# Performance work log

Measured on AMD Instinct MI355X. Metric: run time of the kernel, lower is better.

## Reference

```python
import jax, jax.numpy as jnp
import numpy as np

B, H, W, C = 64, 32, 32, 384          # batch, spatial resolution, channels
NH, WS = 12, 7                        # num_heads, window_size
HD = C // NH                          # head_dim = key_dim (attn_ratio=1)
MLP_H = 4 * C                         # mlp_ratio=4
SCALE = HD ** -0.5
EPS = 1e-5


def _bias_idxs():
    # replicate Attention.__init__ relative-position index construction
    pts = [(i, j) for i in range(WS) for j in range(WS)]
    offs, idxs = {}, []
    for p1 in pts:
        for p2 in pts:
            o = (abs(p1[0] - p2[0]), abs(p1[1] - p2[1]))
            if o not in offs:
                offs[o] = len(offs)
            idxs.append(offs[o])
    return np.array(idxs, dtype=np.int32).reshape(WS * WS, WS * WS), len(offs)


def setup_inputs() -> dict:
    key = jax.random.key(0)
    ks = jax.random.split(key, 8)
    idxs, n_off = _bias_idxs()
    s = lambda k, shape: jax.random.normal(k, shape, jnp.float32) * 0.02
    return {
        'x': jax.random.normal(ks[0], (B, H * W, C), jnp.float32),
        'ln1_g': jnp.ones((C,), jnp.float32), 'ln1_b': jnp.zeros((C,), jnp.float32),
        'qkv_w': s(ks[1], (C, 3 * C)), 'qkv_b': jnp.zeros((3 * C,), jnp.float32),
        'proj_w': s(ks[2], (C, C)), 'proj_b': jnp.zeros((C,), jnp.float32),
        'attn_biases': s(ks[3], (NH, n_off)),
        'conv_w': s(ks[4], (C, 1, 3, 3)),
        'bn_g': jnp.ones((C,), jnp.float32), 'bn_b': jnp.zeros((C,), jnp.float32),
        'bn_m': jnp.zeros((C,), jnp.float32), 'bn_v': jnp.ones((C,), jnp.float32),
        'ln2_g': jnp.ones((C,), jnp.float32), 'ln2_b': jnp.zeros((C,), jnp.float32),
        'fc1_w': s(ks[5], (C, MLP_H)), 'fc1_b': jnp.zeros((MLP_H,), jnp.float32),
        'fc2_w': s(ks[6], (MLP_H, C)), 'fc2_b': jnp.zeros((C,), jnp.float32),
        'bias_idxs': jnp.asarray(idxs),
    }


def _ln(x, g, b):
    m = x.mean(-1, keepdims=True)
    v = ((x - m) ** 2).mean(-1, keepdims=True)
    return (x - m) * jax.lax.rsqrt(v + EPS) * g + b


def _block(x, ln1_g, ln1_b, qkv_w, qkv_b, proj_w, proj_b, attn_biases,
           conv_w, bn_g, bn_b, bn_m, bn_v, ln2_g, ln2_b,
           fc1_w, fc1_b, fc2_w, fc2_b, bias_idxs):
    Bb, L, Cc = x.shape
    res = x
    # ---- window partition with padding ----
    xi = x.reshape(Bb, H, W, Cc)
    pad_b = (WS - H % WS) % WS
    pad_r = (WS - W % WS) % WS
    xi = jnp.pad(xi, ((0, 0), (0, pad_b), (0, pad_r), (0, 0)))
    pH, pW = H + pad_b, W + pad_r
    nHw, nWw = pH // WS, pW // WS
    xw = (xi.reshape(Bb, nHw, WS, nWw, WS, Cc)
            .transpose(0, 1, 3, 2, 4, 5)
            .reshape(Bb * nHw * nWw, WS * WS, Cc))
    # ---- windowed attention with gathered relative-position bias ----
    Bw, N, _ = xw.shape
    xn = _ln(xw, ln1_g, ln1_b)
    qkv = (xn @ qkv_w + qkv_b).reshape(Bw, N, NH, 3 * HD)
    q, k, v = jnp.split(qkv, 3, axis=-1)              # each [Bw, N, NH, HD]
    ab = attn_biases[:, bias_idxs]                     # gather -> [NH, N, N]
    attn = jnp.einsum('bnhd,bmhd->bhnm', q, k) * SCALE + ab
    attn = jax.nn.softmax(attn, axis=-1)
    aw = jnp.einsum('bhnm,bmhd->bnhd', attn, v).reshape(Bw, N, Cc)
    aw = aw @ proj_w + proj_b
    # ---- window merge / unpad ----
    xi = (aw.reshape(Bb, nHw, nWw, WS, WS, Cc)
            .transpose(0, 1, 3, 2, 4, 5)
            .reshape(Bb, pH, pW, Cc))[:, :H, :W]
    x = res + xi.reshape(Bb, L, Cc)
    # ---- depthwise 3x3 conv + BN (eval semantics), NCHW ----
    xc = x.transpose(0, 2, 1).reshape(Bb, Cc, H, W)
    xc = jax.lax.conv_general_dilated(xc, conv_w, (1, 1), ((1, 1), (1, 1)),
                                      feature_group_count=Cc)
    xc = ((xc - bn_m[:, None, None]) * jax.lax.rsqrt(bn_v[:, None, None] + 1e-5)
          * bn_g[:, None, None] + bn_b[:, None, None])
    x = xc.reshape(Bb, Cc, L).transpose(0, 2, 1)
    # ---- MLP (LayerNorm -> fc1 -> GELU -> fc2), residual ----
    h = jax.nn.gelu(_ln(x, ln2_g, ln2_b) @ fc1_w + fc1_b, approximate=False)
    return x + (h @ fc2_w + fc2_b)


def reference(x, ln1_g, ln1_b, qkv_w, qkv_b, proj_w, proj_b, attn_biases,
              conv_w, bn_g, bn_b, bn_m, bn_v, ln2_g, ln2_b,
              fc1_w, fc1_b, fc2_w, fc2_b, bias_idxs):
    return _block(x, ln1_g, ln1_b, qkv_w, qkv_b, proj_w, proj_b, attn_biases,
                  conv_w, bn_g, bn_b, bn_m, bn_v, ln2_g, ln2_b,
                  fc1_w, fc1_b, fc2_w, fc2_b, bias_idxs)
```

## Files before the change

### kernel.cpp

```cpp
#include <hip/hip_runtime.h>
#include <hip/hip_bf16.h>
#include <math.h>

#define NHEAD 12
#define CDIM 384
#define QKVC 1152
#define MLPH 1536
#define SCALE 0.17677669529663687f

typedef __attribute__((ext_vector_type(8))) short short8;
typedef __attribute__((ext_vector_type(4))) float f32x4;

static __device__ __forceinline__ unsigned short f2bf(float f) {
  union { __hip_bfloat16 b; unsigned short u; } c;
  c.b = __float2bfloat16(f);
  return c.u;
}

static __device__ __forceinline__ float gelu_f(float x) {
  float x3 = x * x * x;
  float y = 0.7978845608028654f * (x + 0.044715f * x3);
  float e = __expf(2.f * y);
  float th = 1.f - 2.f / (e + 1.f);
  return 0.5f * x * (1.f + th);
}

__global__ void pad_qkv_kernel(const float* __restrict__ lb, const float* __restrict__ Wq,
                               const float* __restrict__ bq, __hip_bfloat16* __restrict__ outp) {
  int j = blockIdx.x * blockDim.x + threadIdx.x;
  if (j >= QKVC) return;
  float s = bq[j];
  for (int c = 0; c < CDIM; c++) s += lb[c] * Wq[(size_t)c * QKVC + j];
  outp[j] = __float2bfloat16(s);
}

__global__ void expand_bias(const float* __restrict__ biases, const int* __restrict__ bidx,
                            float* __restrict__ Bexp, int n_off) {
  int h = blockIdx.x;
  for (int e = threadIdx.x; e < 4096; e += 256) {
    int n = e >> 6, m = e & 63;
    float v;
    if (m >= 49) v = -1e30f;
    else if (n >= 49) v = 0.f;
    else v = biases[h * n_off + bidx[n * 49 + m]];
    Bexp[h * 4096 + e] = v;
  }
}

__global__ void wt_convert(const float* __restrict__ W, __hip_bfloat16* __restrict__ Wt,
                           int K, int N) {
  __shared__ float t[32][33];
  int n0 = blockIdx.x * 32, k0 = blockIdx.y * 32;
  int tx = threadIdx.x, ty = threadIdx.y;
#pragma unroll
  for (int i = 0; i < 4; i++) t[ty + i * 8][tx] = W[(size_t)(k0 + ty + i * 8) * N + n0 + tx];
  __syncthreads();
#pragma unroll
  for (int i = 0; i < 4; i++)
    Wt[(size_t)(n0 + ty + i * 8) * K + k0 + tx] = __float2bfloat16(t[tx][ty + i * 8]);
}

__global__ void wfragq(const float* __restrict__ W, unsigned short* __restrict__ WF) {
  int f = blockIdx.x;
  int lane = threadIdx.x;
  int kk = f % 12, G = f / 12;
  int n = G * 16 + (lane & 15);
  int k = kk * 32 + (lane >> 4) * 8;
  unsigned short* dst = WF + ((size_t)f * 64 + lane) * 8;
#pragma unroll
  for (int j = 0; j < 8; j++) dst[j] = f2bf(W[(size_t)(k + j) * QKVC + n]);
}

__global__ void wfrag1(const float* __restrict__ W, unsigned short* __restrict__ WF) {
  int f = blockIdx.x;
  int lane = threadIdx.x;
  int wn = f & 7, kk = (f >> 3) % 12, ks = f / 96;
  int n = ks * 128 + wn * 16 + (lane & 15);
  int k = kk * 32 + (lane >> 4) * 8;
  unsigned short* dst = WF + ((size_t)f * 64 + lane) * 8;
#pragma unroll
  for (int j = 0; j < 8; j++) dst[j] = f2bf(W[(size_t)(k + j) * MLPH + n]);
}

__global__ void wfrag2(const float* __restrict__ W, unsigned short* __restrict__ WF) {
  int f = blockIdx.x;
  int lane = threadIdx.x;
  int j = f % 3, wn = (f / 3) & 7, kk = (f / 24) & 3, ks = f / 96;
  int n = wn * 48 + j * 16 + (lane & 15);
  int k = ks * 128 + kk * 32 + (lane >> 4) * 8;
  unsigned short* dst = WF + ((size_t)f * 64 + lane) * 8;
#pragma unroll
  for (int jj = 0; jj < 8; jj++) dst[jj] = f2bf(W[(size_t)(k + jj) * CDIM + n]);
}

__global__ __launch_bounds__(512) void ln_qkv(
    const float* __restrict__ X, const float* __restrict__ g, const float* __restrict__ b,
    const unsigned short* __restrict__ WQF, const float* __restrict__ BQ,
    __hip_bfloat16* __restrict__ QKV) {
  __shared__ unsigned short Al[64][388];
  int tid = threadIdx.x;
  int m0 = blockIdx.x * 64;
  int wave = tid >> 6, lane = tid & 63;
  int l15 = lane & 15, l4 = lane >> 4;

#pragma unroll
  for (int r8 = 0; r8 < 8; r8++) {
    int row = wave * 8 + r8;
    const float* xr = X + (size_t)(m0 + row) * CDIM;
    float vals[6];
    float s = 0.f;
#pragma unroll
    for (int i = 0; i < 6; i++) { vals[i] = xr[lane + i * 64]; s += vals[i]; }
#pragma unroll
    for (int o = 32; o > 0; o >>= 1) s += __shfl_xor(s, o);
    float mean = s * (1.f / 384.f);
    float vs = 0.f;
#pragma unroll
    for (int i = 0; i < 6; i++) { float d = vals[i] - mean; vs += d * d; }
#pragma unroll
    for (int o = 32; o > 0; o >>= 1) vs += __shfl_xor(vs, o);
    float rs = rsqrtf(vs * (1.f / 384.f) + 1e-5f);
#pragma unroll
    for (int i = 0; i < 6; i++) {
      int c = lane + i * 64;
      Al[row][c] = f2bf((vals[i] - mean) * rs * g[c] + b[c]);
    }
  }
  __syncthreads();

  for (int rd = 0; rd < 9; rd++) {
    int G = rd * 8 + wave;
    f32x4 acc[4] = {};
    const unsigned short* wb = WQF + (size_t)(G * 12) * 512 + lane * 8;
#pragma unroll
    for (int kk = 0; kk < 12; kk++) {
      short8 bf = *(const short8*)(wb + kk * 512);
#pragma unroll
      for (int i = 0; i < 4; i++) {
        short8 af = *(const short8*)&Al[i * 16 + l15][kk * 32 + l4 * 8];
        acc[i] = __builtin_amdgcn_mfma_f32_16x16x32_bf16(af, bf, acc[i], 0, 0, 0);
      }
    }
    int n = G * 16 + l15;
    float bv = BQ[n];
    __hip_bfloat16* dst = QKV + (size_t)m0 * QKVC + n;
#pragma unroll
    for (int i = 0; i < 4; i++)
#pragma unroll
      for (int r = 0; r < 4; r++)
        dst[(size_t)(i * 16 + l4 * 4 + r) * QKVC] = __float2bfloat16(acc[i][r] + bv);
  }
}

template <int GELU, int HAS_RES, int OUT_BF16>
__global__ __launch_bounds__(256) void gemm_mfma(
    const __hip_bfloat16* __restrict__ A, const __hip_bfloat16* __restrict__ Bt,
    const float* __restrict__ bias, const float* __restrict__ res,
    void* __restrict__ Cout, int M, int N, int K) {
  __shared__ unsigned short Al[128][72];
  __shared__ unsigned short Bl[64][72];
  int tid = threadIdx.x;
  int m0 = blockIdx.y * 128, n0 = blockIdx.x * 64;
  int wave = tid >> 6, lane = tid & 63;
  int wm = (wave >> 1) * 64, wn = (wave & 1) * 32;
  int l15 = lane & 15, l4 = lane >> 4;

  int am = tid >> 1, ak = (tid & 1) * 32;
  int bn = tid >> 2, bk = (tid & 3) * 16;
  const __hip_bfloat16* Ag = A + (size_t)(m0 + am) * K + ak;
  const __hip_bfloat16* Bg = Bt + (size_t)(n0 + bn) * K + bk;

  f32x4 acc[4][2] = {};

  for (int kt = 0; kt < K; kt += 64) {
    uint4 av0 = *(const uint4*)(Ag + kt);
    uint4 av1 = *(const uint4*)(Ag + kt + 8);
    uint4 av2 = *(const uint4*)(Ag + kt + 16);
    uint4 av3 = *(const uint4*)(Ag + kt + 24);
    uint4 bv0 = *(const uint4*)(Bg + kt);
    uint4 bv1 = *(const uint4*)(Bg + kt + 8);
    __syncthreads();
    *(uint4*)&Al[am][ak]      = av0;
    *(uint4*)&Al[am][ak + 8]  = av1;
    *(uint4*)&Al[am][ak + 16] = av2;
    *(uint4*)&Al[am][ak + 24] = av3;
    *(uint4*)&Bl[bn][bk]      = bv0;
    *(uint4*)&Bl[bn][bk + 8]  = bv1;
    __syncthreads();
#pragma unroll
    for (int kk = 0; kk < 64; kk += 32) {
      short8 af[4], bfr[2];
#pragma unroll
      for (int i = 0; i < 4; i++)
        af[i] = *(const short8*)&Al[wm + i * 16 + l15][kk + l4 * 8];
#pragma unroll
      for (int j = 0; j < 2; j++)
        bfr[j] = *(const short8*)&Bl[wn + j * 16 + l15][kk + l4 * 8];
#pragma unroll
      for (int i = 0; i < 4; i++)
#pragma unroll
        for (int j = 0; j < 2; j++)
          acc[i][j] = __builtin_amdgcn_mfma_f32_16x16x32_bf16(af[i], bfr[j], acc[i][j], 0, 0, 0);
    }
  }

#pragma unroll
  for (int i = 0; i < 4; i++) {
#pragma unroll
    for (int j = 0; j < 2; j++) {
      int n = n0 + wn + j * 16 + l15;
      float bv = bias[n];
#pragma unroll
      for (int r = 0; r < 4; r++) {
        int m = m0 + wm + i * 16 + l4 * 4 + r;
        float c = acc[i][j][r] + bv;
        if (GELU) c = gelu_f(c);
        if (HAS_RES) c += res[(size_t)m * N + n];
        if (OUT_BF16)
          ((__hip_bfloat16*)Cout)[(size_t)m * N + n] = __float2bfloat16(c);
        else
          ((float*)Cout)[(size_t)m * N + n] = c;
      }
    }
  }
}

__global__ __launch_bounds__(512, 4) void mlp_fused(
    const __hip_bfloat16* __restrict__ XN, const unsigned short* __restrict__ W1F,
    const float* __restrict__ B1, const unsigned short* __restrict__ W2F,
    const float* __restrict__ B2, const __hip_bfloat16* __restrict__ X2,
    float* __restrict__ OUT) {
  __shared__ unsigned short XNl[64][388];
  __shared__ unsigned short Hl[64][132];
  int tid = threadIdx.x;
  int m0 = blockIdx.x * 64;
  int wave = tid >> 6, lane = tid & 63;
  int wn = wave;
  int l15 = lane & 15, l4 = lane >> 4;

  {
#pragma unroll
    for (int i = 0; i < 6; i++) {
      int u = tid + i * 512;
      int r = u / 48, col = (u % 48) * 8;
      *(uint4*)&XNl[r][col] =
          *(const uint4*)((const unsigned short*)XN + (size_t)(m0 + r) * 384 + col);
    }
  }

  f32x4 acc[4][3] = {};
  __syncthreads();

  for (int ks = 0; ks < 12; ks++) {
    f32x4 hacc[4] = {};
    const unsigned short* w1fb = W1F + ((size_t)(ks * 96 + wn)) * 512 + lane * 8;
#pragma unroll
    for (int kk = 0; kk < 12; kk++) {
      short8 bf0 = *(const short8*)(w1fb + kk * 4096);
#pragma unroll
      for (int i = 0; i < 4; i++) {
        short8 af = *(const short8*)&XNl[i * 16 + l15][kk * 32 + l4 * 8];
        hacc[i] = __builtin_amdgcn_mfma_f32_16x16x32_bf16(af, bf0, hacc[i], 0, 0, 0);
      }
    }
    float b1v = B1[ks * 128 + wn * 16 + l15];
    __syncthreads();
#pragma unroll
    for (int i = 0; i < 4; i++)
#pragma unroll
      for (int r = 0; r < 4; r++) {
        float c = hacc[i][r] + b1v;
        Hl[i * 16 + l4 * 4 + r][wn * 16 + l15] = f2bf(gelu_f(c));
      }
    __syncthreads();
    const unsigned short* w2fb = W2F + ((size_t)(ks * 96 + wn * 3)) * 512 + lane * 8;
#pragma unroll
    for (int kk = 0; kk < 4; kk++) {
      short8 af2[4];
#pragma unroll
      for (int i = 0; i < 4; i++)
        af2[i] = *(const short8*)&Hl[i * 16 + l15][kk * 32 + l4 * 8];
#pragma unroll
      for (int j = 0; j < 3; j++) {
        short8 bf2 = *(const short8*)(w2fb + kk * 12288 + j * 512);
#pragma unroll
        for (int i = 0; i < 4; i++)
          acc[i][j] = __builtin_amdgcn_mfma_f32_16x16x32_bf16(af2[i], bf2, acc[i][j], 0, 0, 0);
      }
    }
  }
#pragma unroll
  for (int j = 0; j < 3; j++) {
    int n = wn * 48 + j * 16 + l15;
    float bv = B2[n];
#pragma unroll
    for (int i = 0; i < 4; i++)
#pragma unroll
      for (int r = 0; r < 4; r++) {
        int m = m0 + i * 16 + l4 * 4 + r;
        OUT[(size_t)m * 384 + n] =
            acc[i][j][r] + bv + __bfloat162float(X2[(size_t)m * 384 + n]);
      }
  }
}

__global__ __launch_bounds__(64) void attn_mfma(
    const __hip_bfloat16* __restrict__ qkv, const __hip_bfloat16* __restrict__ qkv_pad,
    const float* __restrict__ Bexp, __hip_bfloat16* __restrict__ aw) {
  int h = blockIdx.x % NHEAD;
  int w = blockIdx.x / NHEAD;
  int b = w / 25, wi = w % 25;
  int wh = wi / 5, wv = wi % 5;

  __shared__ unsigned short Q[64][40];
  __shared__ unsigned short K[64][40];
  __shared__ unsigned short Vt[32][72];
  __shared__ unsigned short P[64][72];

  int lane = threadIdx.x;
  int l15 = lane & 15, l4 = lane >> 4;

  {
    int t = lane;
    uint4 z = {0, 0, 0, 0};
    uint4 qv[4], kv[4];
    union { uint4 u[4]; unsigned short s[32]; } vu;
    bool use = t < 49;
    const unsigned short* src = (const unsigned short*)qkv_pad + h * 96;
    if (use) {
      int hh = wh * 7 + t / 7, ww = wv * 7 + t % 7;
      if (hh < 32 && ww < 32)
        src = (const unsigned short*)qkv + (size_t)(b * 1024 + hh * 32 + ww) * QKVC + h * 96;
    }
#pragma unroll
    for (int c = 0; c < 4; c++) {
      qv[c]   = use ? *(const uint4*)(src + c * 8)      : z;
      kv[c]   = use ? *(const uint4*)(src + 32 + c * 8) : z;
      vu.u[c] = use ? *(const uint4*)(src + 64 + c * 8) : z;
    }
#pragma unroll
    for (int c = 0; c < 4; c++) {
      *(uint4*)&Q[t][c * 8] = qv[c];
      *(uint4*)&K[t][c * 8] = kv[c];
    }
#pragma unroll
    for (int d = 0; d < 32; d++) Vt[d][t] = vu.s[d];
  }
  __syncthreads();

  f32x4 acc[4][4] = {};
  {
    short8 aq[4], bk[4];
#pragma unroll
    for (int i = 0; i < 4; i++) aq[i] = *(const short8*)&Q[i * 16 + l15][l4 * 8];
#pragma unroll
    for (int j = 0; j < 4; j++) bk[j] = *(const short8*)&K[j * 16 + l15][l4 * 8];
#pragma unroll
    for (int i = 0; i < 4; i++)
#pragma unroll
      for (int j = 0; j < 4; j++)
        acc[i][j] = __builtin_amdgcn_mfma_f32_16x16x32_bf16(aq[i], bk[j], acc[i][j], 0, 0, 0);
  }

  const float* Bh = Bexp + h * 4096;
  float rinv_[4][4];
#pragma unroll
  for (int i = 0; i < 4; i++) {
    float s[4][4];
#pragma unroll
    for (int j = 0; j < 4; j++)
#pragma unroll
      for (int r = 0; r < 4; r++) {
        int n = i * 16 + l4 * 4 + r, m = j * 16 + l15;
        s[j][r] = acc[i][j][r] * SCALE + Bh[n * 64 + m];
      }
#pragma unroll
    for (int r = 0; r < 4; r++) {
      float mx = fmaxf(fmaxf(s[0][r], s[1][r]), fmaxf(s[2][r], s[3][r]));
#pragma unroll
      for (int o = 1; o < 16; o <<= 1) mx = fmaxf(mx, __shfl_xor(mx, o));
      float p[4], sm = 0.f;
#pragma unroll
      for (int j = 0; j < 4; j++) { p[j] = __expf(s[j][r] - mx); sm += p[j]; }
#pragma unroll
      for (int o = 1; o < 16; o <<= 1) sm += __shfl_xor(sm, o);
      rinv_[i][r] = 1.f / sm;
      int n = i * 16 + l4 * 4 + r;
#pragma unroll
      for (int j = 0; j < 4; j++) P[n][j * 16 + l15] = f2bf(p[j]);
    }
  }
  __syncthreads();

  f32x4 o[4][2] = {};
#pragma unroll
  for (int ks = 0; ks < 2; ks++) {
    short8 pa[4], vb[2];
#pragma unroll
    for (int i = 0; i < 4; i++) pa[i] = *(const short8*)&P[i * 16 + l15][ks * 32 + l4 * 8];
#pragma unroll
    for (int j = 0; j < 2; j++) vb[j] = *(const short8*)&Vt[j * 16 + l15][ks * 32 + l4 * 8];
#pragma unroll
    for (int i = 0; i < 4; i++)
#pragma unroll
      for (int j = 0; j < 2; j++)
        o[i][j] = __builtin_amdgcn_mfma_f32_16x16x32_bf16(pa[i], vb[j], o[i][j], 0, 0, 0);
  }

#pragma unroll
  for (int i = 0; i < 4; i++)
#pragma unroll
    for (int r = 0; r < 4; r++) {
      int n = i * 16 + l4 * 4 + r;
      if (n < 49) {
        int hh = wh * 7 + n / 7, ww = wv * 7 + n % 7;
        if (hh < 32 && ww < 32) {
          __hip_bfloat16* dst = aw + (size_t)(b * 1024 + hh * 32 + ww) * CDIM + h * 32;
          float ri = rinv_[i][r];
#pragma unroll
          for (int j = 0; j < 2; j++)
            dst[j * 16 + l15] = __float2bfloat16(o[i][j][r] * ri);
        }
      }
    }
}

__global__ __launch_bounds__(384) void conv_bn_ln_kernel(
    const __hip_bfloat16* __restrict__ X, const float* __restrict__ W9,
    const float* __restrict__ g, const float* __restrict__ bb,
    const float* __restrict__ mm, const float* __restrict__ vv,
    const float* __restrict__ lg, const float* __restrict__ lb,
    __hip_bfloat16* __restrict__ X2, __hip_bfloat16* __restrict__ XN) {
  int nwg = gridDim.x;
  int id = blockIdx.x;
  int nid = (id & 7) * (nwg >> 3) + (id >> 3);
  int yh = nid & 1;
  int x = (nid >> 1) & 31;
  int b = nid >> 6;
  int c = threadIdx.x;

  float w[9];
#pragma unroll
  for (int i = 0; i < 9; i++) w[i] = W9[c * 9 + i];
  float bnsc = rsqrtf(vv[c] + 1e-5f) * g[c];
  float bnsh = bb[c] - mm[c] * bnsc;
  float lgc = lg[c], lbc = lb[c];

  bool xm = x > 0, xp = x < 31;
  const __hip_bfloat16* colbase = X + ((size_t)(b * 1024 + x)) * CDIM + c;

  __shared__ float part[2][6][2];
  int wv = threadIdx.x >> 6, ln = threadIdx.x & 63;

  float w0[3], w1[3], w2[3];
  int y0 = yh * 16;
  if (y0 == 0) {
    w0[0] = w0[1] = w0[2] = 0.f;
  } else {
    const __hip_bfloat16* p = colbase + (size_t)(y0 - 1) * 32 * CDIM;
    w0[0] = xm ? __bfloat162float(p[-CDIM]) : 0.f;
    w0[1] = __bfloat162float(p[0]);
    w0[2] = xp ? __bfloat162float(p[CDIM]) : 0.f;
  }
  {
    const __hip_bfloat16* p = colbase + (size_t)y0 * 32 * CDIM;
    w1[0] = xm ? __bfloat162float(p[-CDIM]) : 0.f;
    w1[1] = __bfloat162float(p[0]);
    w1[2] = xp ? __bfloat162float(p[CDIM]) : 0.f;
  }

  for (int y = y0; y < y0 + 16; y++) {
    if (y + 1 < 32) {
      const __hip_bfloat16* p = colbase + (size_t)(y + 1) * 32 * CDIM;
      w2[0] = xm ? __bfloat162float(p[-CDIM]) : 0.f;
      w2[1] = __bfloat162float(p[0]);
      w2[2] = xp ? __bfloat162float(p[CDIM]) : 0.f;
    } else {
      w2[0] = w2[1] = w2[2] = 0.f;
    }
    float acc = w0[0] * w[0] + w0[1] * w[1] + w0[2] * w[2]
              + w1[0] * w[3] + w1[1] * w[4] + w1[2] * w[5]
              + w2[0] * w[6] + w2[1] * w[7] + w2[2] * w[8];
    float r = acc * bnsc + bnsh;
    size_t tok = (size_t)(b * 1024 + y * 32 + x);
    X2[tok * CDIM + c] = __float2bfloat16(r);

    float s1 = r, s2 = r * r;
#pragma unroll
    for (int o = 32; o > 0; o >>= 1) { s1 += __shfl_xor(s1, o); s2 += __shfl_xor(s2, o); }
    int pb = y & 1;
    if (ln == 0) { part[pb][wv][0] = s1; part[pb][wv][1] = s2; }
    __syncthreads();
    float ts1 = 0.f, ts2 = 0.f;
#pragma unroll
    for (int i = 0; i < 6; i++) { ts1 += part[pb][i][0]; ts2 += part[pb][i][1]; }
    float mean = ts1 * (1.f / 384.f);
    float var = ts2 * (1.f / 384.f) - mean * mean;
    float rstd = rsqrtf(var + 1e-5f);
    XN[tok * CDIM + c] = __float2bfloat16((r - mean) * rstd * lgc + lbc);

    w0[0] = w1[0]; w0[1] = w1[1]; w0[2] = w1[2];
    w1[0] = w2[0]; w1[1] = w2[1]; w1[2] = w2[2];
  }
}

extern "C" void kernel_launch(void* const* d_in, const int* in_sizes, int n_in,
                              void* d_out, int out_size, void* d_ws, size_t ws_size,
                              hipStream_t stream) {
  const float* x      = (const float*)d_in[0];
  const float* ln1_g  = (const float*)d_in[1];
  const float* ln1_b  = (const float*)d_in[2];
  const float* qkv_w  = (const float*)d_in[3];
  const float* qkv_b  = (const float*)d_in[4];
  const float* proj_w = (const float*)d_in[5];
  const float* proj_b = (const float*)d_in[6];
  const float* att_b  = (const float*)d_in[7];
  const float* conv_w = (const float*)d_in[8];
  const float* bn_g   = (const float*)d_in[9];
  const float* bn_b   = (const float*)d_in[10];
  const float* bn_m   = (const float*)d_in[11];
  const float* bn_v   = (const float*)d_in[12];
  const float* ln2_g  = (const float*)d_in[13];
  const float* ln2_b  = (const float*)d_in[14];
  const float* fc1_w  = (const float*)d_in[15];
  const float* fc1_b  = (const float*)d_in[16];
  const float* fc2_w  = (const float*)d_in[17];
  const float* fc2_b  = (const float*)d_in[18];
  const int* bias_idxs = (const int*)d_in[19];
  int n_off = in_sizes[7] / NHEAD;
  float* out = (float*)d_out;

  char* ws = (char*)d_ws;
  size_t off = 0;
  __hip_bfloat16* qkv_pad = (__hip_bfloat16*)(ws + off); off += QKVC * 2;
  off = (off + 255) & ~(size_t)255;
  float* Bexp = (float*)(ws + off); off += (size_t)NHEAD * 4096 * 4;
  unsigned short* wqf = (unsigned short*)(ws + off); off += (size_t)QKVC * CDIM * 2;
  __hip_bfloat16* wprojT = (__hip_bfloat16*)(ws + off); off += (size_t)CDIM * CDIM * 2;
  unsigned short* w1f = (unsigned short*)(ws + off); off += (size_t)MLPH * CDIM * 2;
  unsigned short* w2f = (unsigned short*)(ws + off); off += (size_t)CDIM * MLPH * 2;
  size_t HDR = (off + 255) & ~(size_t)255;

  const size_t PER_TOK = 4608;
  int Bc = 64;
  while (Bc > 1 && HDR + (size_t)Bc * 1024 * PER_TOK > ws_size) Bc >>= 1;
  size_t Tc = (size_t)Bc * 1024;

  off = HDR;
  __hip_bfloat16* xn = (__hip_bfloat16*)(ws + off); off += Tc * CDIM * 2;
  __hip_bfloat16* qkv = (__hip_bfloat16*)(ws + off); off += Tc * QKVC * 2;
  __hip_bfloat16* x1 = qkv;
  __hip_bfloat16* awb = (__hip_bfloat16*)(ws + off); off += Tc * CDIM * 2;
  __hip_bfloat16* x2 = (__hip_bfloat16*)(ws + off); off += Tc * CDIM * 2;

  pad_qkv_kernel<<<dim3(5), dim3(256), 0, stream>>>(ln1_b, qkv_w, qkv_b, qkv_pad);
  expand_bias<<<dim3(NHEAD), dim3(256), 0, stream>>>(att_b, bias_idxs, Bexp, n_off);
  wfragq<<<dim3(864), dim3(64), 0, stream>>>(qkv_w, wqf);
  wt_convert<<<dim3(CDIM / 32, CDIM / 32), dim3(32, 8), 0, stream>>>(proj_w, wprojT, CDIM, CDIM);
  wfrag1<<<dim3(1152), dim3(64), 0, stream>>>(fc1_w, w1f);
  wfrag2<<<dim3(1152), dim3(64), 0, stream>>>(fc2_w, w2f);

  for (int b0 = 0; b0 < 64; b0 += Bc) {
    const float* xa = x + (size_t)b0 * 1024 * CDIM;
    float* outa = out + (size_t)b0 * 1024 * CDIM;
    int M = (int)Tc;

    ln_qkv<<<dim3(M / 64), dim3(512), 0, stream>>>(xa, ln1_g, ln1_b, wqf, qkv_b, qkv);
    attn_mfma<<<dim3(Bc * 25 * NHEAD), dim3(64), 0, stream>>>(qkv, qkv_pad, Bexp, awb);
    gemm_mfma<0, 1, 1><<<dim3(CDIM / 64, M / 128), dim3(256), 0, stream>>>(
        awb, wprojT, proj_b, xa, x1, M, CDIM, CDIM);
    conv_bn_ln_kernel<<<dim3(Bc * 64), dim3(384), 0, stream>>>(
        x1, conv_w, bn_g, bn_b, bn_m, bn_v, ln2_g, ln2_b, x2, xn);
    mlp_fused<<<dim3(M / 64), dim3(512), 0, stream>>>(
        xn, w1f, fc1_b, w2f, fc2_b, x2, outa);
  }
}
```

Baseline: 762.4 us.

## Replace generic proj GEMM with full-K row-block kernel using pre-fragmented weights

The projection GEMM is rewritten as a dedicated kernel: each 512-thread block loads a 64-row by 384 slab of the attention output into LDS once, then each wave computes three 16-column groups over the full K. The B operand is read directly from a pre-swizzled MFMA fragment layout in global memory. This removes the per-K-tile LDS staging and barriers, and means each A tile is read from global once instead of once per N-tile. The tanh-form GELU helper is also rewritten as an equivalent sigmoid form with fewer operations, though the proj path does not call it.

```diff
diff --git a/kernel.cpp b/kernel.cpp
--- a/kernel.cpp
+++ b/kernel.cpp
@@ -18,11 +18,10 @@
 }
 
 static __device__ __forceinline__ float gelu_f(float x) {
-  float x3 = x * x * x;
-  float y = 0.7978845608028654f * (x + 0.044715f * x3);
-  float e = __expf(2.f * y);
-  float th = 1.f - 2.f / (e + 1.f);
-  return 0.5f * x * (1.f + th);
+  float x2 = x * x;
+  float t = __builtin_fmaf(0.044715f * x2, x, x);
+  float e = __expf(-1.5957691216057308f * t);
+  return x / (1.f + e);
 }
 
 __global__ void pad_qkv_kernel(const float* __restrict__ lb, const float* __restrict__ Wq,
@@ -47,19 +46,6 @@
   }
 }
 
-__global__ void wt_convert(const float* __restrict__ W, __hip_bfloat16* __restrict__ Wt,
-                           int K, int N) {
-  __shared__ float t[32][33];
-  int n0 = blockIdx.x * 32, k0 = blockIdx.y * 32;
-  int tx = threadIdx.x, ty = threadIdx.y;
-#pragma unroll
-  for (int i = 0; i < 4; i++) t[ty + i * 8][tx] = W[(size_t)(k0 + ty + i * 8) * N + n0 + tx];
-  __syncthreads();
-#pragma unroll
-  for (int i = 0; i < 4; i++)
-    Wt[(size_t)(n0 + ty + i * 8) * K + k0 + tx] = __float2bfloat16(t[tx][ty + i * 8]);
-}
-
 __global__ void wfragq(const float* __restrict__ W, unsigned short* __restrict__ WF) {
   int f = blockIdx.x;
   int lane = threadIdx.x;
@@ -69,6 +55,17 @@
   unsigned short* dst = WF + ((size_t)f * 64 + lane) * 8;
 #pragma unroll
   for (int j = 0; j < 8; j++) dst[j] = f2bf(W[(size_t)(k + j) * QKVC + n]);
+}
+
+__global__ void wfragp(const float* __restrict__ W, unsigned short* __restrict__ WF) {
+  int f = blockIdx.x;
+  int lane = threadIdx.x;
+  int kk = f % 12, G = f / 12;
+  int n = G * 16 + (lane & 15);
+  int k = kk * 32 + (lane >> 4) * 8;
+  unsigned short* dst = WF + ((size_t)f * 64 + lane) * 8;
+#pragma unroll
+  for (int j = 0; j < 8; j++) dst[j] = f2bf(W[(size_t)(k + j) * CDIM + n]);
 }
 
 __global__ void wfrag1(const float* __restrict__ W, unsigned short* __restrict__ WF) {
@@ -152,76 +149,55 @@
   }
 }
 
-template <int GELU, int HAS_RES, int OUT_BF16>
-__global__ __launch_bounds__(256) void gemm_mfma(
-    const __hip_bfloat16* __restrict__ A, const __hip_bfloat16* __restrict__ Bt,
-    const float* __restrict__ bias, const float* __restrict__ res,
-    void* __restrict__ Cout, int M, int N, int K) {
-  __shared__ unsigned short Al[128][72];
-  __shared__ unsigned short Bl[64][72];
+__global__ __launch_bounds__(512) void proj_res(
+    const __hip_bfloat16* __restrict__ AW, const unsigned short* __restrict__ WPF,
+    const float* __restrict__ BP, const float* __restrict__ X,
+    __hip_bfloat16* __restrict__ X1) {
+  __shared__ unsigned short Al[64][388];
   int tid = threadIdx.x;
-  int m0 = blockIdx.y * 128, n0 = blockIdx.x * 64;
+  int m0 = blockIdx.x * 64;
   int wave = tid >> 6, lane = tid & 63;
-  int wm = (wave >> 1) * 64, wn = (wave & 1) * 32;
   int l15 = lane & 15, l4 = lane >> 4;
 
-  int am = tid >> 1, ak = (tid & 1) * 32;
-  int bn = tid >> 2, bk = (tid & 3) * 16;
-  const __hip_bfloat16* Ag = A + (size_t)(m0 + am) * K + ak;
-  const __hip_bfloat16* Bg = Bt + (size_t)(n0 + bn) * K + bk;
-
-  f32x4 acc[4][2] = {};
-
-  for (int kt = 0; kt < K; kt += 64) {
-    uint4 av0 = *(const uint4*)(Ag + kt);
-    uint4 av1 = *(const uint4*)(Ag + kt + 8);
-    uint4 av2 = *(const uint4*)(Ag + kt + 16);
-    uint4 av3 = *(const uint4*)(Ag + kt + 24);
-    uint4 bv0 = *(const uint4*)(Bg + kt);
-    uint4 bv1 = *(const uint4*)(Bg + kt + 8);
-    __syncthreads();
-    *(uint4*)&Al[am][ak]      = av0;
-    *(uint4*)&Al[am][ak + 8]  = av1;
-    *(uint4*)&Al[am][ak + 16] = av2;
-    *(uint4*)&Al[am][ak + 24] = av3;
-    *(uint4*)&Bl[bn][bk]      = bv0;
-    *(uint4*)&Bl[bn][bk + 8]  = bv1;
-    __syncthreads();
-#pragma unroll
-    for (int kk = 0; kk < 64; kk += 32) {
-      short8 af[4], bfr[2];
+  {
+#pragma unroll
+    for (int i = 0; i < 6; i++) {
+      int u = tid + i * 512;
+      int r = u / 48, col = (u % 48) * 8;
+      *(uint4*)&Al[r][col] =
+          *(const uint4*)((const unsigned short*)AW + (size_t)(m0 + r) * 384 + col);
+    }
+  }
+  __syncthreads();
+
+  f32x4 acc[4][3] = {};
+#pragma unroll
+  for (int kk = 0; kk < 12; kk++) {
+    short8 af[4];
+#pragma unroll
+    for (int i = 0; i < 4; i++)
+      af[i] = *(const short8*)&Al[i * 16 + l15][kk * 32 + l4 * 8];
+#pragma unroll
+    for (int j = 0; j < 3; j++) {
+      int G = wave * 3 + j;
+      short8 bf = *(const short8*)(WPF + (size_t)(G * 12 + kk) * 512 + lane * 8);
 #pragma unroll
       for (int i = 0; i < 4; i++)
-        af[i] = *(const short8*)&Al[wm + i * 16 + l15][kk + l4 * 8];
-#pragma unroll
-      for (int j = 0; j < 2; j++)
-        bfr[j] = *(const short8*)&Bl[wn + j * 16 + l15][kk + l4 * 8];
-#pragma unroll
-      for (int i = 0; i < 4; i++)
-#pragma unroll
-        for (int j = 0; j < 2; j++)
-          acc[i][j] = __builtin_amdgcn_mfma_f32_16x16x32_bf16(af[i], bfr[j], acc[i][j], 0, 0, 0);
-    }
-  }
-
-#pragma unroll
-  for (int i = 0; i < 4; i++) {
-#pragma unroll
-    for (int j = 0; j < 2; j++) {
-      int n = n0 + wn + j * 16 + l15;
-      float bv = bias[n];
+        acc[i][j] = __builtin_amdgcn_mfma_f32_16x16x32_bf16(af[i], bf, acc[i][j], 0, 0, 0);
+    }
+  }
+#pragma unroll
+  for (int j = 0; j < 3; j++) {
+    int n = (wave * 3 + j) * 16 + l15;
+    float bv = BP[n];
+#pragma unroll
+    for (int i = 0; i < 4; i++)
 #pragma unroll
       for (int r = 0; r < 4; r++) {
-        int m = m0 + wm + i * 16 + l4 * 4 + r;
-        float c = acc[i][j][r] + bv;
-        if (GELU) c = gelu_f(c);
-        if (HAS_RES) c += res[(size_t)m * N + n];
-        if (OUT_BF16)
-          ((__hip_bfloat16*)Cout)[(size_t)m * N + n] = __float2bfloat16(c);
-        else
-          ((float*)Cout)[(size_t)m * N + n] = c;
-      }
-    }
+        int m = m0 + i * 16 + l4 * 4 + r;
+        X1[(size_t)m * 384 + n] =
+            __float2bfloat16(acc[i][j][r] + bv + X[(size_t)m * 384 + n]);
+      }
   }
 }
 
@@ -536,7 +512,7 @@
   off = (off + 255) & ~(size_t)255;
   float* Bexp = (float*)(ws + off); off += (size_t)NHEAD * 4096 * 4;
   unsigned short* wqf = (unsigned short*)(ws + off); off += (size_t)QKVC * CDIM * 2;
-  __hip_bfloat16* wprojT = (__hip_bfloat16*)(ws + off); off += (size_t)CDIM * CDIM * 2;
+  unsigned short* wpf = (unsigned short*)(ws + off); off += (size_t)CDIM * CDIM * 2;
   unsigned short* w1f = (unsigned short*)(ws + off); off += (size_t)MLPH * CDIM * 2;
   unsigned short* w2f = (unsigned short*)(ws + off); off += (size_t)CDIM * MLPH * 2;
   size_t HDR = (off + 255) & ~(size_t)255;
@@ -556,7 +532,7 @@
   pad_qkv_kernel<<<dim3(5), dim3(256), 0, stream>>>(ln1_b, qkv_w, qkv_b, qkv_pad);
   expand_bias<<<dim3(NHEAD), dim3(256), 0, stream>>>(att_b, bias_idxs, Bexp, n_off);
   wfragq<<<dim3(864), dim3(64), 0, stream>>>(qkv_w, wqf);
-  wt_convert<<<dim3(CDIM / 32, CDIM / 32), dim3(32, 8), 0, stream>>>(proj_w, wprojT, CDIM, CDIM);
+  wfragp<<<dim3(288), dim3(64), 0, stream>>>(proj_w, wpf);
   wfrag1<<<dim3(1152), dim3(64), 0, stream>>>(fc1_w, w1f);
   wfrag2<<<dim3(1152), dim3(64), 0, stream>>>(fc2_w, w2f);
 
@@ -567,8 +543,7 @@
 
     ln_qkv<<<dim3(M / 64), dim3(512), 0, stream>>>(xa, ln1_g, ln1_b, wqf, qkv_b, qkv);
     attn_mfma<<<dim3(Bc * 25 * NHEAD), dim3(64), 0, stream>>>(qkv, qkv_pad, Bexp, awb);
-    gemm_mfma<0, 1, 1><<<dim3(CDIM / 64, M / 128), dim3(256), 0, stream>>>(
-        awb, wprojT, proj_b, xa, x1, M, CDIM, CDIM);
+    proj_res<<<dim3(M / 64), dim3(512), 0, stream>>>(awb, wpf, proj_b, xa, x1);
     conv_bn_ln_kernel<<<dim3(Bc * 64), dim3(384), 0, stream>>>(
         x1, conv_w, bn_g, bn_b, bn_m, bn_v, ln2_g, ln2_b, x2, xn);
     mlp_fused<<<dim3(M / 64), dim3(512), 0, stream>>>(
```

Result: no change. 759.9 us (-0.3%).
